# Kernel optimization log

Hardware: AMD Instinct MI355X
Metric: run time of the kernel (lower is better)

The kernel has to match this reference:

```python
import jax, jax.numpy as jnp
import numpy as np

N = 100000      # nodes
E = 1600000     # edges (avg degree 16)
G = 1000        # graphs in batch
F_IN = 128      # num_features
C = 10          # num_classes
EPS = 1e-5


def setup_inputs() -> dict:
    key = jax.random.key(0)
    ks = jax.random.split(key, 12)
    w = lambda k, shape: jax.random.normal(k, shape, jnp.float32) * 0.05
    return {
        'x': jax.random.normal(ks[0], (N, F_IN), jnp.float32),
        'edge_index': jax.random.randint(ks[1], (2, E), 0, N, jnp.int32),
        'edge_weights': jax.random.randint(ks[2], (E,), 0, 2, jnp.int32),
        'batch': jnp.sort(jax.random.randint(ks[3], (N,), 0, G, jnp.int32)),
        'num_graphs': G,
        # initial MLP: Linear(128,32)+BN+ReLU, Linear(32,32)+BN+ReLU
        'W1': w(ks[4], (F_IN, 32)), 'b1': jnp.zeros(32), 'g1': jnp.ones(32), 'bt1': jnp.zeros(32),
        'W2': w(ks[5], (32, 32)), 'b2': jnp.zeros(32), 'g2': jnp.ones(32), 'bt2': jnp.zeros(32),
        'Wl0': w(ks[6], (32, C)), 'bl0': jnp.zeros(C),   # initial_linear
        'Wg1': w(ks[7], (32, 64)), 'bg1': jnp.zeros(64),  # GCNConv 1
        'Wl1': w(ks[8], (64, C)), 'bl1': jnp.zeros(C),
        'Wg2': w(ks[9], (64, 64)), 'bg2': jnp.zeros(64),  # GCNConv 2
        'Wl2': w(ks[10], (64, C)), 'bl2': jnp.zeros(C),
    }


def _bn(h, gamma, beta):
    # BatchNorm1d in training mode: biased batch statistics over nodes
    mu = h.mean(0)
    var = ((h - mu) ** 2).mean(0)
    return gamma * (h - mu) * jax.lax.rsqrt(var + EPS) + beta


def _gcn(h_in, row, col, w, W, b):
    # PyG GCNConv with self-loops: D^{-1/2}(A+I)D^{-1/2} X W + b,
    # edges with mask weight 0 contribute nothing (incl. to degree).
    n = h_in.shape[0]
    h = h_in @ W
    deg = jax.ops.segment_sum(w, col, num_segments=n) + 1.0  # +1 self-loop
    dinv = jax.lax.rsqrt(deg)
    norm = w * dinv[row] * dinv[col]                  # [E]
    agg = jax.ops.segment_sum(h[row] * norm[:, None], col, num_segments=n)
    agg = agg + h * (dinv * dinv)[:, None]            # self-loop term
    return agg + b


def _pool_max(h, batch, num_graphs):
    # torch_scatter scatter_max readout; empty segments -> 0
    p = jax.ops.segment_max(h, batch, num_segments=num_graphs)
    return jnp.where(jnp.isfinite(p), p, 0.0)


def reference(x, edge_index, edge_weights, batch, num_graphs,
              W1, b1, g1, bt1, W2, b2, g2, bt2, Wl0, bl0,
              Wg1, bg1, Wl1, bl1, Wg2, bg2, Wl2, bl2):
    row, col = edge_index[0], edge_index[1]
    w = (edge_weights == 1).astype(x.dtype)  # boolean edge mask as 0/1 weight
    # initial MLP (dropout treated as identity for deterministic reference)
    h = jax.nn.relu(_bn(x @ W1 + b1, g1, bt1))
    h = jax.nn.relu(_bn(h @ W2 + b2, g2, bt2))
    out = _pool_max(h @ Wl0 + bl0, batch, num_graphs)
    # layer 1
    h = _gcn(h, row, col, w, Wg1, bg1)
    out = out + _pool_max(h, batch, num_graphs) @ Wl1 + bl1
    # layer 2
    h = _gcn(h, row, col, w, Wg2, bg2)
    out = out + _pool_max(h, batch, num_graphs) @ Wl2 + bl2
    return out
```

## Files before the change

### kernel.cpp

```cpp
#include <hip/hip_runtime.h>

#define NN 100000
#define EE 1600000
#define GG 1000
#define BN_EPS 1e-5f
#define NB1 391

__device__ __forceinline__ unsigned encf(float f){
  unsigned u = __float_as_uint(f);
  return (u & 0x80000000u) ? ~u : (u | 0x80000000u);
}
__device__ __forceinline__ float dec0(unsigned e){
  unsigned u = (e & 0x80000000u) ? (e & 0x7fffffffu) : ~e;
  float f = __uint_as_float(u);
  return isfinite(f) ? f : 0.0f;
}

__global__ void k_count(const int* __restrict__ ei, const int* __restrict__ ew,
                        int* __restrict__ cnt){
  int e = blockIdx.x*256 + threadIdx.x;
  if (e < EE && ew[e] == 1) atomicAdd(&cnt[ei[EE + e]], 1);
}

__global__ __launch_bounds__(256) void k_scan1(const int* __restrict__ cnt,
    int* __restrict__ loc, int* __restrict__ bsum){
  __shared__ int sm[256];
  const int i = blockIdx.x*256 + threadIdx.x;
  const int v = (i < NN) ? cnt[i] : 0;
  sm[threadIdx.x] = v;
  __syncthreads();
  for (int off = 1; off < 256; off <<= 1){
    int t = (threadIdx.x >= off) ? sm[threadIdx.x - off] : 0;
    __syncthreads();
    sm[threadIdx.x] += t;
    __syncthreads();
  }
  if (i < NN) loc[i] = sm[threadIdx.x] - v;
  if (threadIdx.x == 255) bsum[blockIdx.x] = sm[255];
}

__global__ __launch_bounds__(512) void k_scan2(const int* __restrict__ bsum,
    int* __restrict__ boff){
  __shared__ int sm[512];
  const int t = threadIdx.x;
  const int v = (t < NB1) ? bsum[t] : 0;
  sm[t] = v;
  __syncthreads();
  for (int off = 1; off < 512; off <<= 1){
    int x = (t >= off) ? sm[t - off] : 0;
    __syncthreads();
    sm[t] += x;
    __syncthreads();
  }
  if (t <= NB1) boff[t] = sm[t] - v;
}

__global__ void k_fin(const int* __restrict__ cnt, const int* __restrict__ loc,
                      const int* __restrict__ boff, float* __restrict__ dinv,
                      int* __restrict__ rowstart, int* __restrict__ fill){
  const int i = blockIdx.x*256 + threadIdx.x;
  if (i < NN){
    int rs = loc[i] + boff[i >> 8];
    rowstart[i] = rs; fill[i] = rs;
    dinv[i] = rsqrtf((float)cnt[i] + 1.0f);
  } else if (i == NN){
    rowstart[NN] = boff[NB1];
  }
}

__global__ void k_scatter(const int* __restrict__ ei, const int* __restrict__ ew,
                          int* __restrict__ fill, int* __restrict__ csr){
  int e = blockIdx.x*256 + threadIdx.x;
  if (e < EE && ew[e] == 1){
    int c = ei[EE + e];
    int pos = atomicAdd(&fill[c], 1);
    csr[pos] = ei[e];
  }
}

__global__ __launch_bounds__(256) void k_gemm1(const float* __restrict__ x,
    const float* __restrict__ W1, const float* __restrict__ b1,
    float* __restrict__ Y1, float* __restrict__ stats){
  __shared__ float xs[32*132];
  __shared__ float Ws[128*32];
  __shared__ float red[64];
  const int tid = threadIdx.x;
  for (int j = tid; j < 1024; j += 256) ((float4*)Ws)[j] = ((const float4*)W1)[j];
  const int r = tid >> 3, cg = tid & 7;
  const float4 bv = ((const float4*)b1)[cg];
  float s0=0,s1=0,s2=0,s3=0,q0=0,q1=0,q2=0,q3=0;
  for (int tile = blockIdx.x; tile < 3125; tile += gridDim.x){
    __syncthreads();
    for (int j = tid; j < 1024; j += 256){
      int rr = j >> 5, kk = j & 31;
      *(float4*)&xs[rr*132 + kk*4] = ((const float4*)x)[(size_t)tile*1024 + j];
    }
    __syncthreads();
    float a0=bv.x, a1=bv.y, a2=bv.z, a3=bv.w;
    const float* xr = &xs[r*132];
    const float* wc = &Ws[cg*4];
    #pragma unroll 8
    for (int k = 0; k < 128; k++){
      float xv = xr[k];
      float4 w = *(const float4*)&wc[k*32];
      a0 += xv*w.x; a1 += xv*w.y; a2 += xv*w.z; a3 += xv*w.w;
    }
    float4 o; o.x=a0; o.y=a1; o.z=a2; o.w=a3;
    ((float4*)Y1)[(size_t)(tile*32 + r)*8 + cg] = o;
    s0+=a0; s1+=a1; s2+=a2; s3+=a3;
    q0+=a0*a0; q1+=a1*a1; q2+=a2*a2; q3+=a3*a3;
  }
  __syncthreads();
  if (tid < 64) red[tid] = 0.f;
  __syncthreads();
  atomicAdd(&red[cg*4+0], s0); atomicAdd(&red[cg*4+1], s1);
  atomicAdd(&red[cg*4+2], s2); atomicAdd(&red[cg*4+3], s3);
  atomicAdd(&red[32+cg*4+0], q0); atomicAdd(&red[32+cg*4+1], q1);
  atomicAdd(&red[32+cg*4+2], q2); atomicAdd(&red[32+cg*4+3], q3);
  __syncthreads();
  if (tid < 64) atomicAdd(&stats[tid], red[tid]);
}

__global__ void k_stats(float* __restrict__ stats, const float* __restrict__ gamma,
                        const float* __restrict__ beta, int base){
  int c = threadIdx.x;
  float mean = stats[base + c] * (1.0f/NN);
  float var  = stats[base + 32 + c] * (1.0f/NN) - mean*mean;
  float sc = gamma[c] * rsqrtf(fmaxf(var, 0.0f) + BN_EPS);
  stats[base + 64 + c] = sc;
  stats[base + 96 + c] = beta[c] - mean*sc;
}

__global__ __launch_bounds__(256) void k_mlp2(const float* __restrict__ Y1,
    const float* __restrict__ W2, const float* __restrict__ b2,
    float* __restrict__ stats, float* __restrict__ Y2){
  __shared__ float hs[32*36];
  __shared__ float Ws[32*32];
  __shared__ float red[64];
  const int tid = threadIdx.x;
  ((float4*)Ws)[tid] = ((const float4*)W2)[tid];
  const int r = tid >> 3, cg = tid & 7;
  const float4 bv = ((const float4*)b2)[cg];
  const float4 sc = ((const float4*)(stats + 64))[cg];
  const float4 sh = ((const float4*)(stats + 96))[cg];
  float s0=0,s1=0,s2=0,s3=0,q0=0,q1=0,q2=0,q3=0;
  for (int tile = blockIdx.x; tile < 3125; tile += gridDim.x){
    __syncthreads();
    {
      float4 v = ((const float4*)Y1)[(size_t)tile*256 + tid];
      v.x = fmaxf(fmaf(v.x, sc.x, sh.x), 0.f);
      v.y = fmaxf(fmaf(v.y, sc.y, sh.y), 0.f);
      v.z = fmaxf(fmaf(v.z, sc.z, sh.z), 0.f);
      v.w = fmaxf(fmaf(v.w, sc.w, sh.w), 0.f);
      *(float4*)&hs[r*36 + cg*4] = v;
    }
    __syncthreads();
    float a0=bv.x, a1=bv.y, a2=bv.z, a3=bv.w;
    const float* hr = &hs[r*36];
    const float* wc = &Ws[cg*4];
    #pragma unroll
    for (int k = 0; k < 32; k++){
      float h = hr[k];
      float4 w = *(const float4*)&wc[k*32];
      a0 += h*w.x; a1 += h*w.y; a2 += h*w.z; a3 += h*w.w;
    }
    float4 o; o.x=a0; o.y=a1; o.z=a2; o.w=a3;
    ((float4*)Y2)[(size_t)(tile*32 + r)*8 + cg] = o;
    s0+=a0; s1+=a1; s2+=a2; s3+=a3;
    q0+=a0*a0; q1+=a1*a1; q2+=a2*a2; q3+=a3*a3;
  }
  __syncthreads();
  if (tid < 64) red[tid] = 0.f;
  __syncthreads();
  atomicAdd(&red[cg*4+0], s0); atomicAdd(&red[cg*4+1], s1);
  atomicAdd(&red[cg*4+2], s2); atomicAdd(&red[cg*4+3], s3);
  atomicAdd(&red[32+cg*4+0], q0); atomicAdd(&red[32+cg*4+1], q1);
  atomicAdd(&red[32+cg*4+2], q2); atomicAdd(&red[32+cg*4+3], q3);
  __syncthreads();
  if (tid < 64) atomicAdd(&stats[128 + tid], red[tid]);
}

__global__ __launch_bounds__(256) void k_layer0(const float* __restrict__ Y2,
    const float* __restrict__ stats, const float* __restrict__ Wg1,
    const float* __restrict__ Wl0, const float* __restrict__ bl0,
    const int* __restrict__ batch,
    float* __restrict__ Hg1, unsigned* __restrict__ Pool0){
  __shared__ float hs[32*36];
  __shared__ float Wg[32*64];
  __shared__ float Wl[320];
  __shared__ float bl[10];
  const int tid = threadIdx.x;
  ((float4*)Wg)[tid]       = ((const float4*)Wg1)[tid];
  ((float4*)Wg)[tid + 256] = ((const float4*)Wg1)[tid + 256];
  for (int j = tid; j < 320; j += 256) Wl[j] = Wl0[j];
  if (tid < 10)  bl[tid] = bl0[tid];
  {
    const int rr = tid >> 3, kk = tid & 7;
    const float4 sc = ((const float4*)(stats + 192))[kk];
    const float4 sh = ((const float4*)(stats + 224))[kk];
    float4 v = ((const float4*)Y2)[(size_t)blockIdx.x*256 + tid];
    v.x = fmaxf(fmaf(v.x, sc.x, sh.x), 0.f);
    v.y = fmaxf(fmaf(v.y, sc.y, sh.y), 0.f);
    v.z = fmaxf(fmaf(v.z, sc.z, sh.z), 0.f);
    v.w = fmaxf(fmaf(v.w, sc.w, sh.w), 0.f);
    *(float4*)&hs[rr*36 + kk*4] = v;
  }
  __syncthreads();
  const int w = tid >> 6, f = tid & 63;
  for (int i = 0; i < 8; i++){
    const int r = w*8 + i;
    const int row = blockIdx.x*32 + r;
    const float* hr = &hs[r*36];
    float acc = 0.f;
    #pragma unroll
    for (int k = 0; k < 32; k++) acc += hr[k]*Wg[k*64 + f];
    Hg1[(size_t)row*64 + f] = acc;
    if (f < 10){
      float p = bl[f];
      #pragma unroll
      for (int k = 0; k < 32; k++) p += hr[k]*Wl[k*10 + f];
      atomicMax(&Pool0[batch[row]*10 + f], encf(p));
    }
  }
}

template<bool STORE>
__global__ __launch_bounds__(256) void k_agg(const float* __restrict__ H,
    const float* __restrict__ dinv, const int* __restrict__ rowstart,
    const int* __restrict__ csr, const float* __restrict__ bias,
    const int* __restrict__ batch, float* __restrict__ outp,
    unsigned* __restrict__ Pool){
  const int c = blockIdx.x*4 + (threadIdx.x >> 6);
  const int f = threadIdx.x & 63;
  const int s = rowstart[c], e = rowstart[c+1];
  const float dc = dinv[c];
  float accn = 0.f;
  int j = s;
  for (; j + 1 < e; j += 2){
    int r0 = csr[j], r1 = csr[j+1];
    float d0 = dinv[r0], d1 = dinv[r1];
    accn += H[(size_t)r0*64 + f]*d0;
    accn += H[(size_t)r1*64 + f]*d1;
  }
  if (j < e){ int r = csr[j]; accn += H[(size_t)r*64 + f]*dinv[r]; }
  float h = fmaf(accn, dc, H[(size_t)c*64 + f]*dc*dc) + bias[f];
  if (STORE) outp[(size_t)c*64 + f] = h;
  atomicMax(&Pool[batch[c]*64 + f], encf(h));
}

__global__ __launch_bounds__(256) void k_layer1(const float* __restrict__ H2,
    const float* __restrict__ Wg2, float* __restrict__ Hg2){
  __shared__ float as[32*68];
  __shared__ float Wg[64*64];
  const int tid = threadIdx.x;
  #pragma unroll
  for (int j = 0; j < 4; j++) ((float4*)Wg)[tid + j*256] = ((const float4*)Wg2)[tid + j*256];
  #pragma unroll
  for (int j = 0; j < 2; j++){
    int idx = tid + j*256;
    int rr = idx >> 4, kk = idx & 15;
    *(float4*)&as[rr*68 + kk*4] = ((const float4*)H2)[(size_t)blockIdx.x*512 + idx];
  }
  __syncthreads();
  const int w = tid >> 6, f = tid & 63;
  for (int i = 0; i < 8; i++){
    const int r = w*8 + i;
    const float* ar = &as[r*68];
    float acc = 0.f;
    #pragma unroll
    for (int k = 0; k < 64; k++) acc += ar[k]*Wg[k*64 + f];
    Hg2[(size_t)(blockIdx.x*32 + r)*64 + f] = acc;
  }
}

__global__ __launch_bounds__(256) void k_final(const unsigned* __restrict__ P0,
    const unsigned* __restrict__ P1, const unsigned* __restrict__ P2,
    const float* __restrict__ Wl1, const float* __restrict__ bl1,
    const float* __restrict__ Wl2, const float* __restrict__ bl2,
    float* __restrict__ out){
  const int t = blockIdx.x*256 + threadIdx.x;
  const int g = t >> 4, c = t & 15;
  if (g >= GG || c >= 10) return;
  float acc = dec0(P0[g*10 + c]) + bl1[c] + bl2[c];
  for (int f = 0; f < 64; f++){
    acc += dec0(P1[g*64 + f]) * Wl1[f*10 + c];
    acc += dec0(P2[g*64 + f]) * Wl2[f*10 + c];
  }
  out[g*10 + c] = acc;
}

extern "C" void kernel_launch(void* const* d_in, const int* in_sizes, int n_in,
                              void* d_out, int out_size, void* d_ws, size_t ws_size,
                              hipStream_t stream){
  const float* x   = (const float*)d_in[0];
  const int*   ei  = (const int*)d_in[1];
  const int*   ew  = (const int*)d_in[2];
  const int*   bat = (const int*)d_in[3];
  const float* W1  = (const float*)d_in[5],  *b1  = (const float*)d_in[6];
  const float* g1  = (const float*)d_in[7],  *bt1 = (const float*)d_in[8];
  const float* W2  = (const float*)d_in[9],  *b2  = (const float*)d_in[10];
  const float* g2  = (const float*)d_in[11], *bt2 = (const float*)d_in[12];
  const float* Wl0 = (const float*)d_in[13], *bl0 = (const float*)d_in[14];
  const float* Wg1 = (const float*)d_in[15], *bg1 = (const float*)d_in[16];
  const float* Wl1 = (const float*)d_in[17], *bl1 = (const float*)d_in[18];
  const float* Wg2 = (const float*)d_in[19], *bg2 = (const float*)d_in[20];
  const float* Wl2 = (const float*)d_in[21], *bl2 = (const float*)d_in[22];

  float* ws = (float*)d_ws;
  const size_t oCnt   = 0;
  const size_t oStats = NN;
  const size_t oP0    = oStats + 256;
  const size_t oP1    = oP0 + (size_t)GG*10;
  const size_t oP2    = oP1 + (size_t)GG*64;
  const size_t oZEnd  = oP2 + (size_t)GG*64;
  const size_t oDinv  = oZEnd;
  const size_t oLoc   = oDinv + NN;
  const size_t oBsum  = oLoc + NN;
  const size_t oBoff  = oBsum + 512;
  const size_t oRS    = oBoff + 512;
  const size_t oFill  = oRS + NN + 8;
  const size_t oCsr   = oFill + NN;
  const size_t oA     = oCsr + EE;
  const size_t oB     = oA + (size_t)NN*64;

  int*   cnt   = (int*)(ws + oCnt);
  float* stats = ws + oStats;
  unsigned* P0 = (unsigned*)(ws + oP0);
  unsigned* P1 = (unsigned*)(ws + oP1);
  unsigned* P2 = (unsigned*)(ws + oP2);
  float* dinv  = ws + oDinv;
  int*   loc   = (int*)(ws + oLoc);
  int*   bsum  = (int*)(ws + oBsum);
  int*   boff  = (int*)(ws + oBoff);
  int*   rs    = (int*)(ws + oRS);
  int*   fill  = (int*)(ws + oFill);
  int*   csr   = (int*)(ws + oCsr);
  float* Y1    = ws + oA;
  float* Y2    = ws + oA + (size_t)NN*32;
  float* H2    = ws + oA;
  float* Hg1   = ws + oB;
  float* Hg2   = ws + oB;

  (void)hipMemsetAsync(d_ws, 0, oZEnd*sizeof(float), stream);

  k_count  <<<EE/256, 256, 0, stream>>>(ei, ew, cnt);
  k_scan1  <<<NB1, 256, 0, stream>>>(cnt, loc, bsum);
  k_scan2  <<<1, 512, 0, stream>>>(bsum, boff);
  k_fin    <<<NB1, 256, 0, stream>>>(cnt, loc, boff, dinv, rs, fill);
  k_scatter<<<EE/256, 256, 0, stream>>>(ei, ew, fill, csr);

  k_gemm1<<<512, 256, 0, stream>>>(x, W1, b1, Y1, stats);
  k_stats<<<1, 32, 0, stream>>>(stats, g1, bt1, 0);
  k_mlp2 <<<512, 256, 0, stream>>>(Y1, W2, b2, stats, Y2);
  k_stats<<<1, 32, 0, stream>>>(stats, g2, bt2, 128);
  k_layer0<<<3125, 256, 0, stream>>>(Y2, stats, Wg1, Wl0, bl0, bat, Hg1, P0);
  k_agg<true> <<<NN/4, 256, 0, stream>>>(Hg1, dinv, rs, csr, bg1, bat, H2, P1);
  k_layer1<<<3125, 256, 0, stream>>>(H2, Wg2, Hg2);
  k_agg<false><<<NN/4, 256, 0, stream>>>(Hg2, dinv, rs, csr, bg2, bat, nullptr, P2);
  k_final<<<(GG*16 + 255)/256, 256, 0, stream>>>(P0, P1, P2, Wl1, bl1, Wl2, bl2, (float*)d_out);
}
```

Before: 345.7 us.

## Store GCN features in bf16 and gather four edges per wavefront in aggregation

The transformed node features feeding both GCN aggregations are now written as bf16, which halves the bytes of the random-row gathers. The aggregation kernel is restructured so each wavefront handles four edges at once, with 16 lanes each loading a ushort4, followed by a cross-lane shuffle reduction and vectorised epilogue stores. The grid for the first two MLP GEMM kernels is also tripled. The trade is bf16 rounding error in the aggregated features, and the grid change assumes those kernels stride over rows.

```diff
diff --git a/kernel.cpp b/kernel.cpp
--- a/kernel.cpp
+++ b/kernel.cpp
@@ -14,6 +14,14 @@
   unsigned u = (e & 0x80000000u) ? (e & 0x7fffffffu) : ~e;
   float f = __uint_as_float(u);
   return isfinite(f) ? f : 0.0f;
+}
+__device__ __forceinline__ unsigned short f2bf(float f){
+  unsigned u = __float_as_uint(f);
+  u += 0x7FFFu + ((u >> 16) & 1u);
+  return (unsigned short)(u >> 16);
+}
+__device__ __forceinline__ float bf2f(unsigned short s){
+  return __uint_as_float(((unsigned)s) << 16);
 }
 
 __global__ void k_count(const int* __restrict__ ei, const int* __restrict__ ew,
@@ -184,7 +192,7 @@
     const float* __restrict__ stats, const float* __restrict__ Wg1,
     const float* __restrict__ Wl0, const float* __restrict__ bl0,
     const int* __restrict__ batch,
-    float* __restrict__ Hg1, unsigned* __restrict__ Pool0){
+    unsigned short* __restrict__ Hg1, unsigned* __restrict__ Pool0){
   __shared__ float hs[32*36];
   __shared__ float Wg[32*64];
   __shared__ float Wl[320];
@@ -214,7 +222,7 @@
     float acc = 0.f;
     #pragma unroll
     for (int k = 0; k < 32; k++) acc += hr[k]*Wg[k*64 + f];
-    Hg1[(size_t)row*64 + f] = acc;
+    Hg1[(size_t)row*64 + f] = f2bf(acc);
     if (f < 10){
       float p = bl[f];
       #pragma unroll
@@ -225,31 +233,53 @@
 }
 
 template<bool STORE>
-__global__ __launch_bounds__(256) void k_agg(const float* __restrict__ H,
+__global__ __launch_bounds__(256) void k_agg(const ushort4* __restrict__ Hb,
     const float* __restrict__ dinv, const int* __restrict__ rowstart,
     const int* __restrict__ csr, const float* __restrict__ bias,
     const int* __restrict__ batch, float* __restrict__ outp,
     unsigned* __restrict__ Pool){
+  const int lane = threadIdx.x & 63;
+  const int g = lane >> 4;
+  const int l16 = lane & 15;
   const int c = blockIdx.x*4 + (threadIdx.x >> 6);
-  const int f = threadIdx.x & 63;
   const int s = rowstart[c], e = rowstart[c+1];
-  const float dc = dinv[c];
-  float accn = 0.f;
-  int j = s;
-  for (; j + 1 < e; j += 2){
-    int r0 = csr[j], r1 = csr[j+1];
-    float d0 = dinv[r0], d1 = dinv[r1];
-    accn += H[(size_t)r0*64 + f]*d0;
-    accn += H[(size_t)r1*64 + f]*d1;
-  }
-  if (j < e){ int r = csr[j]; accn += H[(size_t)r*64 + f]*dinv[r]; }
-  float h = fmaf(accn, dc, H[(size_t)c*64 + f]*dc*dc) + bias[f];
-  if (STORE) outp[(size_t)c*64 + f] = h;
-  atomicMax(&Pool[batch[c]*64 + f], encf(h));
+  float a0=0.f, a1=0.f, a2=0.f, a3=0.f;
+  for (int j = s + g; j < e; j += 4){
+    const int r = csr[j];
+    const float dr = dinv[r];
+    ushort4 hv = Hb[(size_t)r*16 + l16];
+    a0 = fmaf(bf2f(hv.x), dr, a0);
+    a1 = fmaf(bf2f(hv.y), dr, a1);
+    a2 = fmaf(bf2f(hv.z), dr, a2);
+    a3 = fmaf(bf2f(hv.w), dr, a3);
+  }
+  a0 += __shfl_xor(a0, 16, 64); a1 += __shfl_xor(a1, 16, 64);
+  a2 += __shfl_xor(a2, 16, 64); a3 += __shfl_xor(a3, 16, 64);
+  a0 += __shfl_xor(a0, 32, 64); a1 += __shfl_xor(a1, 32, 64);
+  a2 += __shfl_xor(a2, 32, 64); a3 += __shfl_xor(a3, 32, 64);
+  if (g == 0){
+    const float dc = dinv[c];
+    const ushort4 hv = Hb[(size_t)c*16 + l16];
+    const float4 bv = ((const float4*)bias)[l16];
+    const float dcc = dc*dc;
+    float h0 = fmaf(a0, dc, fmaf(bf2f(hv.x), dcc, bv.x));
+    float h1 = fmaf(a1, dc, fmaf(bf2f(hv.y), dcc, bv.y));
+    float h2 = fmaf(a2, dc, fmaf(bf2f(hv.z), dcc, bv.z));
+    float h3 = fmaf(a3, dc, fmaf(bf2f(hv.w), dcc, bv.w));
+    if (STORE){
+      float4 o; o.x=h0; o.y=h1; o.z=h2; o.w=h3;
+      ((float4*)outp)[(size_t)c*16 + l16] = o;
+    }
+    const int b = batch[c];
+    atomicMax(&Pool[b*64 + l16*4 + 0], encf(h0));
+    atomicMax(&Pool[b*64 + l16*4 + 1], encf(h1));
+    atomicMax(&Pool[b*64 + l16*4 + 2], encf(h2));
+    atomicMax(&Pool[b*64 + l16*4 + 3], encf(h3));
+  }
 }
 
 __global__ __launch_bounds__(256) void k_layer1(const float* __restrict__ H2,
-    const float* __restrict__ Wg2, float* __restrict__ Hg2){
+    const float* __restrict__ Wg2, unsigned short* __restrict__ Hg2){
   __shared__ float as[32*68];
   __shared__ float Wg[64*64];
   const int tid = threadIdx.x;
@@ -269,7 +299,7 @@
     float acc = 0.f;
     #pragma unroll
     for (int k = 0; k < 64; k++) acc += ar[k]*Wg[k*64 + f];
-    Hg2[(size_t)(blockIdx.x*32 + r)*64 + f] = acc;
+    Hg2[(size_t)(blockIdx.x*32 + r)*64 + f] = f2bf(acc);
   }
 }
 
@@ -321,7 +351,7 @@
   const size_t oFill  = oRS + NN + 8;
   const size_t oCsr   = oFill + NN;
   const size_t oA     = oCsr + EE;
-  const size_t oB     = oA + (size_t)NN*64;
+  const size_t oHgb   = oA + (size_t)NN*64;
 
   int*   cnt   = (int*)(ws + oCnt);
   float* stats = ws + oStats;
@@ -338,8 +368,7 @@
   float* Y1    = ws + oA;
   float* Y2    = ws + oA + (size_t)NN*32;
   float* H2    = ws + oA;
-  float* Hg1   = ws + oB;
-  float* Hg2   = ws + oB;
+  unsigned short* Hgb = (unsigned short*)(ws + oHgb);
 
   (void)hipMemsetAsync(d_ws, 0, oZEnd*sizeof(float), stream);
 
@@ -349,13 +378,13 @@
   k_fin    <<<NB1, 256, 0, stream>>>(cnt, loc, boff, dinv, rs, fill);
   k_scatter<<<EE/256, 256, 0, stream>>>(ei, ew, fill, csr);
 
-  k_gemm1<<<512, 256, 0, stream>>>(x, W1, b1, Y1, stats);
+  k_gemm1<<<1536, 256, 0, stream>>>(x, W1, b1, Y1, stats);
   k_stats<<<1, 32, 0, stream>>>(stats, g1, bt1, 0);
-  k_mlp2 <<<512, 256, 0, stream>>>(Y1, W2, b2, stats, Y2);
+  k_mlp2 <<<1536, 256, 0, stream>>>(Y1, W2, b2, stats, Y2);
   k_stats<<<1, 32, 0, stream>>>(stats, g2, bt2, 128);
-  k_layer0<<<3125, 256, 0, stream>>>(Y2, stats, Wg1, Wl0, bl0, bat, Hg1, P0);
-  k_agg<true> <<<NN/4, 256, 0, stream>>>(Hg1, dinv, rs, csr, bg1, bat, H2, P1);
-  k_layer1<<<3125, 256, 0, stream>>>(H2, Wg2, Hg2);
-  k_agg<false><<<NN/4, 256, 0, stream>>>(Hg2, dinv, rs, csr, bg2, bat, nullptr, P2);
+  k_layer0<<<3125, 256, 0, stream>>>(Y2, stats, Wg1, Wl0, bl0, bat, Hgb, P0);
+  k_agg<true> <<<NN/4, 256, 0, stream>>>((const ushort4*)Hgb, dinv, rs, csr, bg1, bat, H2, P1);
+  k_layer1<<<3125, 256, 0, stream>>>(H2, Wg2, Hgb);
+  k_agg<false><<<NN/4, 256, 0, stream>>>((const ushort4*)Hgb, dinv, rs, csr, bg2, bat, nullptr, P2);
   k_final<<<(GG*16 + 255)/256, 256, 0, stream>>>(P0, P1, P2, Wl1, bl1, Wl2, bl2, (float*)d_out);
 }
```

Result: slower. 425.4 us (+23.0%).
